# Optimization experiments

Hardware: AMD Instinct MI355X
Metric: run time of the kernel (lower is better)

The kernel has to match this reference:

```python
import jax, jax.numpy as jnp
import numpy as np

LEAKY = 0.5      # args.leaky
TEMP = 1.0       # args.temp
N_USER = 100000  # args.user
N_ITEM = 50000   # args.item
LATDIM = 128     # args.latdim
HYPERNUM = 128   # args.hyperNum
N_LAYERS = 2     # args.gnn_layer
N_EDGES = 1000000
BATCH = 4096


def _leaky(x):
    return jnp.maximum(LEAKY * x, x)


def _l2norm(x):
    # torch.nn.functional.normalize(p=2, dim=1): x / max(||x||, 1e-12)
    n = jnp.linalg.norm(x, axis=1, keepdims=True)
    return x / jnp.maximum(n, 1e-12)


def _spmm(rows, cols, vals, x, n_out):
    # torch.sparse.mm(adj, x) with adj given as COO (rows, cols, vals)
    return jax.ops.segment_sum(vals[:, None] * x[cols], rows, num_segments=n_out)


def _hyper_prop(lats, adj, Ws):
    # lats: [N, D], adj: [N, H] (dense hyper adjacency), Ws: [3, H, H]
    lat = _leaky(adj.T @ lats)                    # [H, D]
    for k in range(3):
        # (LeakyRelu(lat.T @ W)).T + lat == LeakyRelu(W.T @ lat) + lat
        lat = _leaky(Ws[k].T @ lat) + lat
    return _leaky(adj @ lat)                      # [N, D]


def _ssl(hyperLat, gnnLat):
    pos = jnp.exp(jnp.sum(hyperLat * gnnLat, axis=1) / TEMP)
    neg = jnp.sum(jnp.exp(gnnLat @ hyperLat.T / TEMP), axis=1)
    return jnp.sum(-jnp.log(pos / (neg + 1e-8) + 1e-8))


def setup_inputs() -> dict:
    key = jax.random.key(0)
    ks = jax.random.split(key, 12)
    # distinct ids so jnp.sort(ids) == torch.unique(ids)
    uids = jax.random.permutation(ks[0], N_USER)[:BATCH].astype(jnp.int32)
    iids = jax.random.permutation(ks[1], N_ITEM)[:BATCH].astype(jnp.int32)
    adj_rows = jax.random.randint(ks[2], (N_EDGES,), 0, N_USER, dtype=jnp.int32)
    adj_cols = jax.random.randint(ks[3], (N_EDGES,), 0, N_ITEM, dtype=jnp.int32)
    adj_vals = jax.random.uniform(ks[4], (N_EDGES,), dtype=jnp.float32)
    s_emb = 0.05
    s_hh = (2.0 / (HYPERNUM + HYPERNUM)) ** 0.5   # xavier_normal
    s_dh = (2.0 / (LATDIM + HYPERNUM)) ** 0.5
    s_dd = (2.0 / (LATDIM + LATDIM)) ** 0.5
    uEmbed0 = jax.random.normal(ks[5], (N_USER, LATDIM), jnp.float32) * s_emb
    iEmbed0 = jax.random.normal(ks[6], (N_ITEM, LATDIM), jnp.float32) * s_emb
    uhyper = jax.random.normal(ks[7], (LATDIM, HYPERNUM), jnp.float32) * s_dh
    ihyper = jax.random.normal(ks[8], (LATDIM, HYPERNUM), jnp.float32) * s_dh
    Wu = jax.random.normal(ks[9], (N_LAYERS, 3, HYPERNUM, HYPERNUM), jnp.float32) * s_hh
    Wi = jax.random.normal(ks[10], (N_LAYERS, 3, HYPERNUM, HYPERNUM), jnp.float32) * s_hh
    Wt = jax.random.normal(ks[11], (N_LAYERS, LATDIM, LATDIM), jnp.float32) * s_dd
    return {"uids": uids, "iids": iids, "adj_rows": adj_rows, "adj_cols": adj_cols,
            "adj_vals": adj_vals, "uEmbed0": uEmbed0, "iEmbed0": iEmbed0,
            "uhyper": uhyper, "ihyper": ihyper, "Wu": Wu, "Wi": Wi, "Wt": Wt}


def reference(uids, iids, adj_rows, adj_cols, adj_vals, uEmbed0, iEmbed0,
              uhyper, ihyper, Wu, Wi, Wt):
    # droprate = 0 => edgeDropout and feature dropout are identity
    uuHyper = uEmbed0 @ uhyper   # [N_USER, H]
    iiHyper = iEmbed0 @ ihyper   # [N_ITEM, H]
    ulats, ilats = [uEmbed0], [iEmbed0]
    gnnU, gnnI, hypU, hypI = [], [], [], []
    for l in range(N_LAYERS):
        ulat = _leaky(_spmm(adj_rows, adj_cols, adj_vals, ilats[-1], N_USER))
        ilat = _leaky(_spmm(adj_cols, adj_rows, adj_vals, ulats[-1], N_ITEM))
        hu = _hyper_prop(ulats[-1], uuHyper, Wu[l])
        hi = _hyper_prop(ilats[-1], iiHyper, Wi[l])
        gnnU.append(ulat); gnnI.append(ilat); hypU.append(hu); hypI.append(hi)
        ulats.append(ulat + hu + ulats[-1])
        ilats.append(ilat + hi + ilats[-1])
    ulat = sum(ulats)
    ilat = sum(ilats)
    preds = jnp.sum(ulat[uids] * ilat[iids], axis=-1)
    uniqU = jnp.sort(uids)  # uids are distinct -> equals torch.unique
    uniqI = jnp.sort(iids)
    ssl = jnp.asarray(0.0, jnp.float32)
    for l in range(N_LAYERS):
        ssl = ssl + _ssl(_l2norm(hypU[l][uniqU]) @ Wt[l], _l2norm(gnnU[l][uniqU]))
        ssl = ssl + _ssl(_l2norm(hypI[l][uniqI]) @ Wt[l], _l2norm(gnnI[l][uniqI]))
    reg = (jnp.sum(jnp.square(uEmbed0)) + jnp.sum(jnp.square(iEmbed0)) +
           jnp.sum(jnp.square(uhyper)) + jnp.sum(jnp.square(ihyper)))
    return preds, ssl, reg
```

## Files before the change

### kernel.cpp

```cpp
#include <hip/hip_runtime.h>

#define NU 100000
#define NI 50000
#define DD 128
#define HH 128
#define NE 1000000
#define NB 4096
#define SCHUNK 2048
#define ATBB 512

__device__ __forceinline__ float lk(float x) { return fmaxf(0.5f * x, x); }

__global__ __launch_bounds__(256) void hist_kernel(const int* __restrict__ idx,
                                                   int* __restrict__ deg, int n) {
  int e = blockIdx.x * 256 + threadIdx.x;
  if (e < n) atomicAdd(&deg[idx[e]], 1);
}

__global__ __launch_bounds__(256) void scan_bsum(const int* __restrict__ deg,
                                                 int* __restrict__ bsum, int N) {
  int b = blockIdx.x, t = threadIdx.x;
  int base = b * SCHUNK;
  int s = 0;
  for (int i = t; i < SCHUNK; i += 256) {
    int g = base + i;
    if (g < N) s += deg[g];
  }
#pragma unroll
  for (int o = 32; o > 0; o >>= 1) s += __shfl_down(s, o);
  __shared__ int ws[4];
  if ((t & 63) == 0) ws[t >> 6] = s;
  __syncthreads();
  if (t == 0) bsum[b] = ws[0] + ws[1] + ws[2] + ws[3];
}

__global__ __launch_bounds__(256) void scan_top(int* __restrict__ bsum, int G) {
  int t = threadIdx.x;
  __shared__ int sh[256];
  int v = (t < G) ? bsum[t] : 0;
  sh[t] = v;
  __syncthreads();
  for (int o = 1; o < 256; o <<= 1) {
    int add = (t >= o) ? sh[t - o] : 0;
    __syncthreads();
    sh[t] += add;
    __syncthreads();
  }
  if (t < G) bsum[t] = sh[t] - v;
}

__global__ __launch_bounds__(256) void scan_write(const int* __restrict__ deg,
                                                  const int* __restrict__ bsumx,
                                                  int* __restrict__ rowptr,
                                                  int* __restrict__ cursor,
                                                  int N, int total) {
  int b = blockIdx.x, t = threadIdx.x;
  int base = b * SCHUNK + t * 8;
  int v[8], s = 0;
#pragma unroll
  for (int i = 0; i < 8; i++) {
    int g = base + i;
    v[i] = (g < N) ? deg[g] : 0;
    s += v[i];
  }
  __shared__ int sh[256];
  sh[t] = s;
  __syncthreads();
  for (int o = 1; o < 256; o <<= 1) {
    int add = (t >= o) ? sh[t - o] : 0;
    __syncthreads();
    sh[t] += add;
    __syncthreads();
  }
  int off = bsumx[b] + sh[t] - s;
#pragma unroll
  for (int i = 0; i < 8; i++) {
    int g = base + i;
    if (g < N) { rowptr[g] = off; cursor[g] = off; }
    off += v[i];
  }
  if (b == 0 && t == 0) rowptr[N] = total;
}

__global__ __launch_bounds__(256) void scatter_kernel(const int* __restrict__ idx,
                                                      const int* __restrict__ other,
                                                      const float* __restrict__ vals,
                                                      int* __restrict__ cursor,
                                                      int* __restrict__ scol,
                                                      float* __restrict__ sval, int n) {
  int e = blockIdx.x * 256 + threadIdx.x;
  if (e < n) {
    int p = atomicAdd(&cursor[idx[e]], 1);
    scol[p] = other[e];
    sval[p] = vals[e];
  }
}

__global__ __launch_bounds__(256) void spmm_csr_kernel(
    const int* __restrict__ rowptr, const int* __restrict__ scol,
    const float* __restrict__ sval, const float* __restrict__ x,
    float* __restrict__ y, int N) {
  int w = (blockIdx.x * 256 + threadIdx.x) >> 6;
  if (w >= N) return;
  int lane = threadIdx.x & 63;
  int half = lane >> 5, l32 = lane & 31;
  const float4* x4 = (const float4*)x;
  int j0 = rowptr[w], j1 = rowptr[w + 1];
  float ax = 0.f, ay = 0.f, az = 0.f, aw = 0.f;
  int j = j0 + half;
  for (; j + 2 < j1; j += 4) {
    int c0 = scol[j], c1 = scol[j + 2];
    float v0 = sval[j], v1 = sval[j + 2];
    float4 x0 = x4[(size_t)c0 * 32 + l32];
    float4 x1 = x4[(size_t)c1 * 32 + l32];
    ax += v0 * x0.x + v1 * x1.x;
    ay += v0 * x0.y + v1 * x1.y;
    az += v0 * x0.z + v1 * x1.z;
    aw += v0 * x0.w + v1 * x1.w;
  }
  for (; j < j1; j += 2) {
    int c0 = scol[j];
    float v0 = sval[j];
    float4 x0 = x4[(size_t)c0 * 32 + l32];
    ax += v0 * x0.x; ay += v0 * x0.y; az += v0 * x0.z; aw += v0 * x0.w;
  }
  ax += __shfl_xor(ax, 32); ay += __shfl_xor(ay, 32);
  az += __shfl_xor(az, 32); aw += __shfl_xor(aw, 32);
  if (half == 0) {
    float4 r; r.x = ax; r.y = ay; r.z = az; r.w = aw;
    ((float4*)y)[(size_t)w * 32 + l32] = r;
  }
}

__global__ __launch_bounds__(256) void atb_kernel(
    const float* __restrict__ E, const float* __restrict__ X,
    float* __restrict__ part, int N) {
  __shared__ __align__(16) float Es[64][132];
  __shared__ __align__(16) float Xs[64][132];
  int t = threadIdx.x;
  int ip = (t >> 4) << 2;
  int jp = (t & 15) << 2;
  int rpb = (N + (int)gridDim.x - 1) / (int)gridDim.x;
  int n0 = blockIdx.x * rpb;
  int n1 = min(n0 + rpb, N);
  float acc[2][2][4][4] = {};
  const float4* E4 = (const float4*)E;
  const float4* X4 = (const float4*)X;
  for (int n = n0; n < n1; n += 64) {
    int nr = min(64, n1 - n);
    __syncthreads();
#pragma unroll
    for (int q = 0; q < 8; q++) {
      int f = t + (q << 8);
      int row = f >> 5, c4 = f & 31;
      float4 ev = {0.f, 0.f, 0.f, 0.f}, xv = {0.f, 0.f, 0.f, 0.f};
      if (row < nr) {
        size_t gi = (size_t)(n + row) * 32 + c4;
        ev = E4[gi]; xv = X4[gi];
      }
      *(float4*)&Es[row][c4 << 2] = ev;
      *(float4*)&Xs[row][c4 << 2] = xv;
    }
    __syncthreads();
#pragma unroll 2
    for (int rr = 0; rr < 64; rr++) {
      float4 e0 = *(const float4*)&Es[rr][ip];
      float4 e1 = *(const float4*)&Es[rr][ip + 64];
      float4 x0 = *(const float4*)&Xs[rr][jp];
      float4 x1 = *(const float4*)&Xs[rr][jp + 64];
      const float* e0p = (const float*)&e0;
      const float* e1p = (const float*)&e1;
      const float* x0p = (const float*)&x0;
      const float* x1p = (const float*)&x1;
#pragma unroll
      for (int ai = 0; ai < 4; ai++)
#pragma unroll
        for (int aj = 0; aj < 4; aj++) {
          acc[0][0][ai][aj] += e0p[ai] * x0p[aj];
          acc[0][1][ai][aj] += e0p[ai] * x1p[aj];
          acc[1][0][ai][aj] += e1p[ai] * x0p[aj];
          acc[1][1][ai][aj] += e1p[ai] * x1p[aj];
        }
    }
  }
  float* dst = part + (size_t)blockIdx.x * 16384;
#pragma unroll
  for (int rh = 0; rh < 2; rh++)
#pragma unroll
    for (int ai = 0; ai < 4; ai++) {
      int row = rh * 64 + ip + ai;
#pragma unroll
      for (int ch = 0; ch < 2; ch++) {
        float4 v;
        v.x = acc[rh][ch][ai][0]; v.y = acc[rh][ch][ai][1];
        v.z = acc[rh][ch][ai][2]; v.w = acc[rh][ch][ai][3];
        *(float4*)&dst[row * 128 + ch * 64 + jp] = v;
      }
    }
}

__global__ __launch_bounds__(256) void reduce_atb_kernel(
    const float* __restrict__ part, float* __restrict__ A) {
  int e4 = blockIdx.x * 256 + threadIdx.x;
  const float4* p4 = (const float4*)part;
  float4 s = {0.f, 0.f, 0.f, 0.f};
#pragma unroll 4
  for (int b = 0; b < ATBB; b++) {
    float4 v = p4[(size_t)b * 4096 + e4];
    s.x += v.x; s.y += v.y; s.z += v.z; s.w += v.w;
  }
  ((float4*)A)[e4] = s;
}

__global__ __launch_bounds__(256) void chain_kernel(
    const float* __restrict__ A_u, const float* __restrict__ A_i,
    const float* __restrict__ uhy, const float* __restrict__ ihy,
    const float* __restrict__ Wu_l, const float* __restrict__ Wi_l,
    float* __restrict__ B_u, float* __restrict__ B_i) {
  __shared__ float Wb[128 * 132];
  __shared__ float LA[128][16];
  __shared__ float LB[128][16];
  int side = blockIdx.x >> 3, strip = blockIdx.x & 7;
  const float* A = side ? A_i : A_u;
  const float* hy = side ? ihy : uhy;
  const float* W = side ? Wi_l : Wu_l;
  float* Bo = side ? B_i : B_u;
  int t = threadIdx.x;
  int j0 = strip * 16;
  for (int i = t; i < 2048; i += 256) LA[i >> 4][i & 15] = A[(i >> 4) * 128 + j0 + (i & 15)];
  for (int i = t; i < 16384; i += 256) Wb[(i >> 7) * 132 + (i & 127)] = hy[i];
  __syncthreads();
  int jc = t & 15, i0 = (t >> 4) * 8;
  {
    float acc[8] = {};
    for (int k = 0; k < 128; k++) {
      float lv = LA[k][jc];
      const float* wr = &Wb[k * 132 + i0];
#pragma unroll
      for (int a = 0; a < 8; a++) acc[a] += wr[a] * lv;
    }
#pragma unroll
    for (int a = 0; a < 8; a++) LB[i0 + a][jc] = lk(acc[a]);
  }
  __syncthreads();
  float (*pin)[16] = LB;
  float (*pout)[16] = LA;
  for (int s = 0; s < 3; s++) {
    for (int i = t; i < 16384; i += 256) Wb[(i >> 7) * 132 + (i & 127)] = W[s * 16384 + i];
    __syncthreads();
    float acc[8] = {};
    for (int k = 0; k < 128; k++) {
      float lv = pin[k][jc];
      const float* wr = &Wb[k * 132 + i0];
#pragma unroll
      for (int a = 0; a < 8; a++) acc[a] += wr[a] * lv;
    }
#pragma unroll
    for (int a = 0; a < 8; a++) pout[i0 + a][jc] = lk(acc[a]) + pin[i0 + a][jc];
    __syncthreads();
    float (*tmp)[16] = pin; pin = pout; pout = tmp;
  }
  for (int i = t; i < 16384; i += 256) Wb[(i >> 7) * 132 + (i & 127)] = hy[i];
  __syncthreads();
  {
    int i = t >> 1, jb = (t & 1) * 8;
    float acc[8] = {};
    for (int k = 0; k < 128; k++) {
      float hv = Wb[i * 132 + k];
      const float* lr = &pin[k][jb];
#pragma unroll
      for (int b = 0; b < 8; b++) acc[b] += hv * lr[b];
    }
#pragma unroll
    for (int b = 0; b < 8; b++) Bo[i * 128 + j0 + jb + b] = acc[b];
  }
}

__global__ __launch_bounds__(512) void nmul_upd_kernel(
    const float* __restrict__ E, const float* __restrict__ Bm,
    const float* __restrict__ gnn, float* __restrict__ cur, int N) {
  __shared__ __align__(16) float Bs[128][128];
  int t = threadIdx.x;
  int dg = t & 15, rg = t >> 4;
  const float4* B4 = (const float4*)Bm;
#pragma unroll
  for (int q = 0; q < 8; q++) {
    int f = t + (q << 9);
    *(float4*)&Bs[f >> 5][(f & 31) << 2] = B4[f];
  }
  __syncthreads();
  int n0 = blockIdx.x << 7;
  const float4* E4 = (const float4*)E;
  float acc[4][8] = {};
  int rows[4];
  bool val[4];
#pragma unroll
  for (int a = 0; a < 4; a++) { rows[a] = n0 + rg + (a << 5); val[a] = rows[a] < N; }
  for (int h4 = 0; h4 < 128; h4 += 4) {
    float4 ev[4];
#pragma unroll
    for (int a = 0; a < 4; a++)
      ev[a] = val[a] ? E4[(size_t)rows[a] * 32 + (h4 >> 2)]
                     : make_float4(0.f, 0.f, 0.f, 0.f);
#pragma unroll
    for (int hh = 0; hh < 4; hh++) {
      float4 b0 = *(const float4*)&Bs[h4 + hh][dg << 2];
      float4 b1 = *(const float4*)&Bs[h4 + hh][(dg << 2) + 64];
#pragma unroll
      for (int a = 0; a < 4; a++) {
        float e = ((const float*)&ev[a])[hh];
        acc[a][0] += e * b0.x; acc[a][1] += e * b0.y;
        acc[a][2] += e * b0.z; acc[a][3] += e * b0.w;
        acc[a][4] += e * b1.x; acc[a][5] += e * b1.y;
        acc[a][6] += e * b1.z; acc[a][7] += e * b1.w;
      }
    }
  }
#pragma unroll
  for (int a = 0; a < 4; a++) {
    if (val[a]) {
      size_t base = (size_t)rows[a] * DD + (dg << 2);
      float4 g0 = *(const float4*)(gnn + base);
      float4 g1 = *(const float4*)(gnn + base + 64);
      float4 c0 = *(const float4*)(cur + base);
      float4 c1 = *(const float4*)(cur + base + 64);
      c0.x += lk(g0.x) + lk(acc[a][0]); c0.y += lk(g0.y) + lk(acc[a][1]);
      c0.z += lk(g0.z) + lk(acc[a][2]); c0.w += lk(g0.w) + lk(acc[a][3]);
      c1.x += lk(g1.x) + lk(acc[a][4]); c1.y += lk(g1.y) + lk(acc[a][5]);
      c1.z += lk(g1.z) + lk(acc[a][6]); c1.w += lk(g1.w) + lk(acc[a][7]);
      *(float4*)(cur + base) = c0; *(float4*)(cur + base + 64) = c1;
    }
  }
}

__global__ __launch_bounds__(128) void sslgath_kernel(
    const int* __restrict__ ids, const float* __restrict__ gnn,
    const float* __restrict__ E, const float* __restrict__ Bm,
    float* __restrict__ og, float* __restrict__ oh) {
  __shared__ __align__(16) float Bs[128][132];
  __shared__ __align__(16) float Eb[32][132];
  __shared__ int idb[32];
  int t = threadIdx.x;
  int base = blockIdx.x * 32;
  if (t < 32) idb[t] = ids[base + t];
#pragma unroll
  for (int q = 0; q < 32; q++) {
    int f = t + q * 128;
    *(float4*)&Bs[f >> 5][(f & 31) << 2] = ((const float4*)Bm)[f];
  }
  __syncthreads();
#pragma unroll
  for (int q = 0; q < 8; q++) {
    int f = t + q * 128;
    int r = f >> 5, c4 = f & 31;
    *(float4*)&Eb[r][c4 << 2] = ((const float4*)E)[(size_t)idb[r] * 32 + c4];
  }
  __syncthreads();
  float acc[32] = {};
  for (int k = 0; k < 128; k++) {
    float b = Bs[k][t];
#pragma unroll
    for (int r = 0; r < 32; r++) acc[r] += Eb[r][k] * b;
  }
  for (int r = 0; r < 32; r++) {
    int id = idb[r];
    og[(size_t)(base + r) * DD + t] = lk(gnn[(size_t)id * DD + t]);
    oh[(size_t)(base + r) * DD + t] = lk(acc[r]);
  }
}

__global__ __launch_bounds__(128) void gaccum_kernel(
    const int* __restrict__ ids, const float* __restrict__ cur,
    float* __restrict__ sumg) {
  int b = blockIdx.x, d = threadIdx.x;
  int id = ids[b];
  sumg[(size_t)b * DD + d] += cur[(size_t)id * DD + d];
}

__global__ __launch_bounds__(256) void preds_kernel(
    const float* __restrict__ su, const float* __restrict__ si,
    float* __restrict__ outp) {
  int gid = blockIdx.x * 256 + threadIdx.x;
  int w = gid >> 6, lane = gid & 63;
  if (w >= NB) return;
  float2 a = *(const float2*)(su + (size_t)w * DD + 2 * lane);
  float2 b = *(const float2*)(si + (size_t)w * DD + 2 * lane);
  float d = a.x * b.x + a.y * b.y;
#pragma unroll
  for (int o = 32; o > 0; o >>= 1) d += __shfl_down(d, o);
  if (lane == 0) outp[w] = d;
}

__global__ __launch_bounds__(256) void sumsq_kernel(
    const float* __restrict__ x, int n, float* __restrict__ outp) {
  float acc = 0.f;
  for (int i = blockIdx.x * 256 + threadIdx.x; i < n; i += gridDim.x * 256) {
    float v = x[i];
    acc += v * v;
  }
#pragma unroll
  for (int o = 32; o > 0; o >>= 1) acc += __shfl_down(acc, o);
  __shared__ float s[4];
  if ((threadIdx.x & 63) == 0) s[threadIdx.x >> 6] = acc;
  __syncthreads();
  if (threadIdx.x == 0) atomicAdd(outp, s[0] + s[1] + s[2] + s[3]);
}

__global__ __launch_bounds__(128) void norm_kernel(
    const float* __restrict__ gh, float* __restrict__ gg,
    float* __restrict__ hn) {
  int r = blockIdx.x, d = threadIdx.x;
  __shared__ float red[4];
  float hv = gh[(size_t)r * DD + d];
  float gv = gg[(size_t)r * DD + d];
  float h2 = hv * hv, g2 = gv * gv;
#pragma unroll
  for (int o = 32; o > 0; o >>= 1) { h2 += __shfl_down(h2, o); g2 += __shfl_down(g2, o); }
  if ((d & 63) == 0) { red[(d >> 6) * 2] = h2; red[(d >> 6) * 2 + 1] = g2; }
  __syncthreads();
  float hnorm = sqrtf(red[0] + red[2]);
  float gnorm = sqrtf(red[1] + red[3]);
  hn[(size_t)r * DD + d] = hv / fmaxf(hnorm, 1e-12f);
  gg[(size_t)r * DD + d] = gv / fmaxf(gnorm, 1e-12f);
}

__global__ __launch_bounds__(256) void nmul_plain_kernel(
    const float* __restrict__ In, const float* __restrict__ Wm,
    float* __restrict__ outp) {
  __shared__ __align__(16) float Bs[128][128];
  int t = threadIdx.x;
  int dg = t & 15, rg = t >> 4;
  const float4* W4 = (const float4*)Wm;
#pragma unroll
  for (int q = 0; q < 16; q++) {
    int f = t + (q << 8);
    *(float4*)&Bs[f >> 5][(f & 31) << 2] = W4[f];
  }
  __syncthreads();
  int n0 = blockIdx.x << 5;
  const float4* I4 = (const float4*)In;
  float acc[2][8] = {};
  for (int h4 = 0; h4 < 128; h4 += 4) {
    float4 ev[2];
#pragma unroll
    for (int a = 0; a < 2; a++)
      ev[a] = I4[(size_t)(n0 + rg + (a << 4)) * 32 + (h4 >> 2)];
#pragma unroll
    for (int hh = 0; hh < 4; hh++) {
      float4 b0 = *(const float4*)&Bs[h4 + hh][dg << 2];
      float4 b1 = *(const float4*)&Bs[h4 + hh][(dg << 2) + 64];
#pragma unroll
      for (int a = 0; a < 2; a++) {
        float e = ((const float*)&ev[a])[hh];
        acc[a][0] += e * b0.x; acc[a][1] += e * b0.y;
        acc[a][2] += e * b0.z; acc[a][3] += e * b0.w;
        acc[a][4] += e * b1.x; acc[a][5] += e * b1.y;
        acc[a][6] += e * b1.z; acc[a][7] += e * b1.w;
      }
    }
  }
#pragma unroll
  for (int a = 0; a < 2; a++) {
    size_t base = (size_t)(n0 + rg + (a << 4)) * DD + (dg << 2);
    float4 v0, v1;
    v0.x = acc[a][0]; v0.y = acc[a][1]; v0.z = acc[a][2]; v0.w = acc[a][3];
    v1.x = acc[a][4]; v1.y = acc[a][5]; v1.z = acc[a][6]; v1.w = acc[a][7];
    *(float4*)(outp + base) = v0;
    *(float4*)(outp + base + 64) = v1;
  }
}

__global__ __launch_bounds__(256) void gram_kernel(
    const float* __restrict__ gn, const float* __restrict__ hw,
    float* __restrict__ neg) {
  __shared__ __align__(16) float Hs[64][128];
  int t = threadIdx.x;
  int rg = t >> 4, dg = t & 15;
  int i0 = blockIdx.x << 7, j0 = blockIdx.y << 6;
  float4* Hs4 = (float4*)Hs;
  const float4* hw4 = (const float4*)hw;
#pragma unroll
  for (int q = 0; q < 8; q++) {
    int f = t + (q << 8);
    int j = f >> 5, k4 = f & 31;
    Hs4[j * 32 + (k4 ^ ((j >> 2) & 7))] = hw4[(size_t)(j0 + j) * 32 + k4];
  }
  __syncthreads();
  const float4* G4 = (const float4*)gn;
  float acc[8][4] = {};
  for (int h4 = 0; h4 < 128; h4 += 4) {
    int k4 = h4 >> 2;
    float4 gv[8];
#pragma unroll
    for (int a = 0; a < 8; a++)
      gv[a] = G4[(size_t)(i0 + rg + (a << 4)) * 32 + k4];
    float4 bv[4];
#pragma unroll
    for (int jj = 0; jj < 4; jj++) {
      int j = (dg << 2) + jj;
      bv[jj] = *(const float4*)&Hs[j][(k4 ^ ((j >> 2) & 7)) << 2];
    }
#pragma unroll
    for (int a = 0; a < 8; a++)
#pragma unroll
      for (int jj = 0; jj < 4; jj++)
        acc[a][jj] += gv[a].x * bv[jj].x + gv[a].y * bv[jj].y +
                      gv[a].z * bv[jj].z + gv[a].w * bv[jj].w;
  }
#pragma unroll
  for (int a = 0; a < 8; a++) {
    float s = expf(acc[a][0]) + expf(acc[a][1]) + expf(acc[a][2]) + expf(acc[a][3]);
    s += __shfl_xor(s, 1);
    s += __shfl_xor(s, 2);
    s += __shfl_xor(s, 4);
    s += __shfl_xor(s, 8);
    if (dg == 0) atomicAdd(&neg[i0 + rg + (a << 4)], s);
  }
}

__global__ __launch_bounds__(256) void sslfin_kernel(
    const float* __restrict__ gn, const float* __restrict__ hw,
    const float* __restrict__ neg, float* __restrict__ outp) {
  int gid = blockIdx.x * 256 + threadIdx.x;
  int w = gid >> 6, lane = gid & 63;
  if (w >= NB) return;
  float2 a = *(const float2*)(gn + (size_t)w * DD + 2 * lane);
  float2 b = *(const float2*)(hw + (size_t)w * DD + 2 * lane);
  float d = a.x * b.x + a.y * b.y;
#pragma unroll
  for (int o = 32; o > 0; o >>= 1) d += __shfl_down(d, o);
  if (lane == 0) {
    float pos = expf(d);
    float v = -logf(pos / (neg[w] + 1e-8f) + 1e-8f);
    atomicAdd(outp, v);
  }
}

extern "C" void kernel_launch(void* const* d_in, const int* in_sizes, int n_in,
                              void* d_out, int out_size, void* d_ws, size_t ws_size,
                              hipStream_t stream) {
  (void)in_sizes; (void)n_in; (void)out_size; (void)ws_size;
  const int* uids = (const int*)d_in[0];
  const int* iids = (const int*)d_in[1];
  const int* arow = (const int*)d_in[2];
  const int* acol = (const int*)d_in[3];
  const float* avals = (const float*)d_in[4];
  const float* uE = (const float*)d_in[5];
  const float* iE = (const float*)d_in[6];
  const float* uhy = (const float*)d_in[7];
  const float* ihy = (const float*)d_in[8];
  const float* Wu = (const float*)d_in[9];
  const float* Wi = (const float*)d_in[10];
  const float* Wt = (const float*)d_in[11];
  float* out = (float*)d_out;

  float* p = (float*)d_ws;
  float* cur_u = p; p += (size_t)NU * DD;
  float* gnn_u = p; p += (size_t)NU * DD;
  float* cur_i = p; p += (size_t)NI * DD;
  float* gnn_i = p; p += (size_t)NI * DD;
  float* A_u = p; p += HH * DD;
  float* A_i = p; p += HH * DD;
  float* B_u = p; p += HH * DD;
  float* B_i = p; p += HH * DD;
  float* sumg_u = p; p += (size_t)NB * DD;
  float* sumg_i = p; p += (size_t)NB * DD;
  float* region = p; p += (size_t)ATBB * 16384;
  float* negb = p; p += 4 * NB;
  int* rowptr_u = (int*)p; p += NU + 1;
  int* cursor_u = (int*)p; p += NU;
  int* rowptr_i = (int*)p; p += NI + 1;
  int* cursor_i = (int*)p; p += NI;
  int* bsum = (int*)p; p += 256;
  int* scol_u = (int*)p; p += NE;
  float* sval_u = p; p += NE;
  int* scol_i = (int*)p; p += NE;
  float* sval_i = p; p += NE;

  float* Apart = region;
  float* gg = region;
  float* gh = region + (size_t)NB * DD;
  float* hn = region + 2 * (size_t)NB * DD;

  const int GU = (NU + SCHUNK - 1) / SCHUNK;
  const int GI = (NI + SCHUNK - 1) / SCHUNK;
  const int EB = (NE + 255) / 256;
  const int TU = (NU + 127) >> 7;
  const int TI = (NI + 127) >> 7;

  hipMemsetAsync(cursor_u, 0, NU * sizeof(int), stream);
  hist_kernel<<<EB, 256, 0, stream>>>(arow, cursor_u, NE);
  scan_bsum<<<GU, 256, 0, stream>>>(cursor_u, bsum, NU);
  scan_top<<<1, 256, 0, stream>>>(bsum, GU);
  scan_write<<<GU, 256, 0, stream>>>(cursor_u, bsum, rowptr_u, cursor_u, NU, NE);
  scatter_kernel<<<EB, 256, 0, stream>>>(arow, acol, avals, cursor_u, scol_u, sval_u, NE);

  hipMemsetAsync(cursor_i, 0, NI * sizeof(int), stream);
  hist_kernel<<<EB, 256, 0, stream>>>(acol, cursor_i, NE);
  scan_bsum<<<GI, 256, 0, stream>>>(cursor_i, bsum, NI);
  scan_top<<<1, 256, 0, stream>>>(bsum, GI);
  scan_write<<<GI, 256, 0, stream>>>(cursor_i, bsum, rowptr_i, cursor_i, NI, NE);
  scatter_kernel<<<EB, 256, 0, stream>>>(acol, arow, avals, cursor_i, scol_i, sval_i, NE);

  hipMemcpyAsync(cur_u, uE, (size_t)NU * DD * 4, hipMemcpyDeviceToDevice, stream);
  hipMemcpyAsync(cur_i, iE, (size_t)NI * DD * 4, hipMemcpyDeviceToDevice, stream);
  hipMemsetAsync(out + NB, 0, 2 * sizeof(float), stream);
  hipMemsetAsync(negb, 0, 4 * NB * sizeof(float), stream);
  hipMemsetAsync(sumg_u, 0, 2 * (size_t)NB * DD * 4, stream);
  gaccum_kernel<<<NB, 128, 0, stream>>>(uids, uE, sumg_u);
  gaccum_kernel<<<NB, 128, 0, stream>>>(iids, iE, sumg_i);

  for (int l = 0; l < 2; l++) {
    const float* Wt_l = Wt + (size_t)l * DD * DD;
    spmm_csr_kernel<<<NU / 4, 256, 0, stream>>>(rowptr_u, scol_u, sval_u, cur_i, gnn_u, NU);
    spmm_csr_kernel<<<NI / 4, 256, 0, stream>>>(rowptr_i, scol_i, sval_i, cur_u, gnn_i, NI);
    atb_kernel<<<ATBB, 256, 0, stream>>>(uE, cur_u, Apart, NU);
    reduce_atb_kernel<<<16, 256, 0, stream>>>(Apart, A_u);
    atb_kernel<<<ATBB, 256, 0, stream>>>(iE, cur_i, Apart, NI);
    reduce_atb_kernel<<<16, 256, 0, stream>>>(Apart, A_i);
    chain_kernel<<<16, 256, 0, stream>>>(A_u, A_i, uhy, ihy,
        Wu + (size_t)l * 3 * HH * HH, Wi + (size_t)l * 3 * HH * HH, B_u, B_i);

    sslgath_kernel<<<NB / 32, 128, 0, stream>>>(uids, gnn_u, uE, B_u, gg, gh);
    nmul_upd_kernel<<<TU, 512, 0, stream>>>(uE, B_u, gnn_u, cur_u, NU);
    gaccum_kernel<<<NB, 128, 0, stream>>>(uids, cur_u, sumg_u);
    norm_kernel<<<NB, 128, 0, stream>>>(gh, gg, hn);
    nmul_plain_kernel<<<NB / 32, 256, 0, stream>>>(hn, Wt_l, gh);
    gram_kernel<<<dim3(NB / 128, NB / 64), 256, 0, stream>>>(gg, gh, negb + (2 * l) * NB);
    sslfin_kernel<<<NB / 4, 256, 0, stream>>>(gg, gh, negb + (2 * l) * NB, out + NB);

    sslgath_kernel<<<NB / 32, 128, 0, stream>>>(iids, gnn_i, iE, B_i, gg, gh);
    nmul_upd_kernel<<<TI, 512, 0, stream>>>(iE, B_i, gnn_i, cur_i, NI);
    gaccum_kernel<<<NB, 128, 0, stream>>>(iids, cur_i, sumg_i);
    norm_kernel<<<NB, 128, 0, stream>>>(gh, gg, hn);
    nmul_plain_kernel<<<NB / 32, 256, 0, stream>>>(hn, Wt_l, gh);
    gram_kernel<<<dim3(NB / 128, NB / 64), 256, 0, stream>>>(gg, gh, negb + (2 * l + 1) * NB);
    sslfin_kernel<<<NB / 4, 256, 0, stream>>>(gg, gh, negb + (2 * l + 1) * NB, out + NB);
  }

  preds_kernel<<<NB / 4, 256, 0, stream>>>(sumg_u, sumg_i, out);
  sumsq_kernel<<<2048, 256, 0, stream>>>(uE, NU * DD, out + NB + 1);
  sumsq_kernel<<<1024, 256, 0, stream>>>(iE, NI * DD, out + NB + 1);
  sumsq_kernel<<<64, 256, 0, stream>>>(uhy, DD * HH, out + NB + 1);
  sumsq_kernel<<<64, 256, 0, stream>>>(ihy, DD * HH, out + NB + 1);
}
```

Baseline: 2.217 ms.

## Merge user/item kernels and fuse hypergraph A^T X reduction into update pass

Batches the user and item variants of spmm, gather, gram, finalize, gaccum and sumsq into single launches indexed by side. The hyper-adjacency projection for layer 0 reads only the input embeddings, so it is computed once up front. The layer-1 projection is fused into the nmul update kernel's tile loop, which saves a separate read of the embeddings and current latents. The norm and Wt matmul kernels are merged. This removes many launches and some memory passes, at the cost of an extra synchronisation and serial per-row accumulation inside the update kernel.

```diff
diff --git a/kernel.cpp b/kernel.cpp
--- a/kernel.cpp
+++ b/kernel.cpp
@@ -7,7 +7,6 @@
 #define NE 1000000
 #define NB 4096
 #define SCHUNK 2048
-#define ATBB 512
 
 __device__ __forceinline__ float lk(float x) { return fmaxf(0.5f * x, x); }
 
@@ -96,11 +95,23 @@
   }
 }
 
-__global__ __launch_bounds__(256) void spmm_csr_kernel(
-    const int* __restrict__ rowptr, const int* __restrict__ scol,
-    const float* __restrict__ sval, const float* __restrict__ x,
-    float* __restrict__ y, int N) {
-  int w = (blockIdx.x * 256 + threadIdx.x) >> 6;
+__global__ __launch_bounds__(256) void spmm_both_kernel(
+    const int* __restrict__ rp_u, const int* __restrict__ sc_u,
+    const float* __restrict__ sv_u, const float* __restrict__ xu,
+    float* __restrict__ yu,
+    const int* __restrict__ rp_i, const int* __restrict__ sc_i,
+    const float* __restrict__ sv_i, const float* __restrict__ xi,
+    float* __restrict__ yi) {
+  int bid = blockIdx.x;
+  const int* rowptr; const int* scol; const float* sval;
+  const float* x; float* y; int N;
+  if (bid < NU / 4) {
+    rowptr = rp_u; scol = sc_u; sval = sv_u; x = xu; y = yu; N = NU;
+  } else {
+    bid -= NU / 4;
+    rowptr = rp_i; scol = sc_i; sval = sv_i; x = xi; y = yi; N = NI;
+  }
+  int w = bid * 4 + (threadIdx.x >> 6);
   if (w >= N) return;
   int lane = threadIdx.x & 63;
   int half = lane >> 5, l32 = lane & 31;
@@ -132,20 +143,20 @@
   }
 }
 
-__global__ __launch_bounds__(256) void atb_kernel(
-    const float* __restrict__ E, const float* __restrict__ X,
-    float* __restrict__ part, int N) {
+__global__ __launch_bounds__(256) void atb0_kernel(
+    const float* __restrict__ uE, const float* __restrict__ iE,
+    float* __restrict__ part) {
+  int side = blockIdx.x >> 8, bid = blockIdx.x & 255;
+  const float* E = side ? iE : uE;
+  int N = side ? NI : NU;
   __shared__ __align__(16) float Es[64][132];
-  __shared__ __align__(16) float Xs[64][132];
   int t = threadIdx.x;
-  int ip = (t >> 4) << 2;
-  int jp = (t & 15) << 2;
-  int rpb = (N + (int)gridDim.x - 1) / (int)gridDim.x;
-  int n0 = blockIdx.x * rpb;
+  int ip = (t >> 4) << 2, jp = (t & 15) << 2;
+  int rpb = (N + 255) >> 8;
+  int n0 = bid * rpb;
   int n1 = min(n0 + rpb, N);
   float acc[2][2][4][4] = {};
   const float4* E4 = (const float4*)E;
-  const float4* X4 = (const float4*)X;
   for (int n = n0; n < n1; n += 64) {
     int nr = min(64, n1 - n);
     __syncthreads();
@@ -153,21 +164,17 @@
     for (int q = 0; q < 8; q++) {
       int f = t + (q << 8);
       int row = f >> 5, c4 = f & 31;
-      float4 ev = {0.f, 0.f, 0.f, 0.f}, xv = {0.f, 0.f, 0.f, 0.f};
-      if (row < nr) {
-        size_t gi = (size_t)(n + row) * 32 + c4;
-        ev = E4[gi]; xv = X4[gi];
-      }
+      float4 ev = {0.f, 0.f, 0.f, 0.f};
+      if (row < nr) ev = E4[(size_t)(n + row) * 32 + c4];
       *(float4*)&Es[row][c4 << 2] = ev;
-      *(float4*)&Xs[row][c4 << 2] = xv;
     }
     __syncthreads();
 #pragma unroll 2
     for (int rr = 0; rr < 64; rr++) {
       float4 e0 = *(const float4*)&Es[rr][ip];
       float4 e1 = *(const float4*)&Es[rr][ip + 64];
-      float4 x0 = *(const float4*)&Xs[rr][jp];
-      float4 x1 = *(const float4*)&Xs[rr][jp + 64];
+      float4 x0 = *(const float4*)&Es[rr][jp];
+      float4 x1 = *(const float4*)&Es[rr][jp + 64];
       const float* e0p = (const float*)&e0;
       const float* e1p = (const float*)&e1;
       const float* x0p = (const float*)&x0;
@@ -199,17 +206,20 @@
     }
 }
 
-__global__ __launch_bounds__(256) void reduce_atb_kernel(
-    const float* __restrict__ part, float* __restrict__ A) {
-  int e4 = blockIdx.x * 256 + threadIdx.x;
-  const float4* p4 = (const float4*)part;
+__global__ __launch_bounds__(256) void reduce_both_kernel(
+    const float* __restrict__ part, float* __restrict__ A_u,
+    float* __restrict__ A_i) {
+  int b = blockIdx.x;
+  int side = b >> 4;
+  int e4 = (b & 15) * 256 + threadIdx.x;
+  const float4* p4 = (const float4*)(part + (size_t)side * 256 * 16384);
   float4 s = {0.f, 0.f, 0.f, 0.f};
 #pragma unroll 4
-  for (int b = 0; b < ATBB; b++) {
-    float4 v = p4[(size_t)b * 4096 + e4];
+  for (int k = 0; k < 256; k++) {
+    float4 v = p4[(size_t)k * 4096 + e4];
     s.x += v.x; s.y += v.y; s.z += v.z; s.w += v.w;
   }
-  ((float4*)A)[e4] = s;
+  ((float4*)(side ? A_i : A_u))[e4] = s;
 }
 
 __global__ __launch_bounds__(256) void chain_kernel(
@@ -276,9 +286,20 @@
   }
 }
 
-__global__ __launch_bounds__(512) void nmul_upd_kernel(
-    const float* __restrict__ E, const float* __restrict__ Bm,
-    const float* __restrict__ gnn, float* __restrict__ cur, int N) {
+template <int DOATB>
+__global__ __launch_bounds__(512) void nmul_atb_kernel(
+    const float* __restrict__ uE, const float* __restrict__ Bu,
+    const float* __restrict__ gu, float* __restrict__ cu,
+    const float* __restrict__ iE, const float* __restrict__ Bi,
+    const float* __restrict__ gi, float* __restrict__ ci,
+    float* __restrict__ part) {
+  int side = blockIdx.x >> 8, bid = blockIdx.x & 255;
+  const float* E = side ? iE : uE;
+  const float* Bm = side ? Bi : Bu;
+  const float* gnn = side ? gi : gu;
+  float* cur = side ? ci : cu;
+  int N = side ? NI : NU;
+  int ntiles = (N + 127) >> 7;
   __shared__ __align__(16) float Bs[128][128];
   int t = threadIdx.x;
   int dg = t & 15, rg = t >> 4;
@@ -289,54 +310,99 @@
     *(float4*)&Bs[f >> 5][(f & 31) << 2] = B4[f];
   }
   __syncthreads();
-  int n0 = blockIdx.x << 7;
+  float atb[4][8] = {};
   const float4* E4 = (const float4*)E;
-  float acc[4][8] = {};
-  int rows[4];
-  bool val[4];
-#pragma unroll
-  for (int a = 0; a < 4; a++) { rows[a] = n0 + rg + (a << 5); val[a] = rows[a] < N; }
-  for (int h4 = 0; h4 < 128; h4 += 4) {
-    float4 ev[4];
-#pragma unroll
-    for (int a = 0; a < 4; a++)
-      ev[a] = val[a] ? E4[(size_t)rows[a] * 32 + (h4 >> 2)]
-                     : make_float4(0.f, 0.f, 0.f, 0.f);
-#pragma unroll
-    for (int hh = 0; hh < 4; hh++) {
-      float4 b0 = *(const float4*)&Bs[h4 + hh][dg << 2];
-      float4 b1 = *(const float4*)&Bs[h4 + hh][(dg << 2) + 64];
-#pragma unroll
-      for (int a = 0; a < 4; a++) {
-        float e = ((const float*)&ev[a])[hh];
-        acc[a][0] += e * b0.x; acc[a][1] += e * b0.y;
-        acc[a][2] += e * b0.z; acc[a][3] += e * b0.w;
-        acc[a][4] += e * b1.x; acc[a][5] += e * b1.y;
-        acc[a][6] += e * b1.z; acc[a][7] += e * b1.w;
+  const float4* C4 = (const float4*)cur;
+  for (int tile = bid; tile < ntiles; tile += 256) {
+    int n0 = tile << 7;
+    float acc[4][8] = {};
+    int rows[4];
+    bool val[4];
+#pragma unroll
+    for (int a = 0; a < 4; a++) { rows[a] = n0 + rg + (a << 5); val[a] = rows[a] < N; }
+    for (int h4 = 0; h4 < 128; h4 += 4) {
+      float4 ev[4];
+#pragma unroll
+      for (int a = 0; a < 4; a++)
+        ev[a] = val[a] ? E4[(size_t)rows[a] * 32 + (h4 >> 2)]
+                       : make_float4(0.f, 0.f, 0.f, 0.f);
+#pragma unroll
+      for (int hh = 0; hh < 4; hh++) {
+        float4 b0 = *(const float4*)&Bs[h4 + hh][dg << 2];
+        float4 b1 = *(const float4*)&Bs[h4 + hh][(dg << 2) + 64];
+#pragma unroll
+        for (int a = 0; a < 4; a++) {
+          float e = ((const float*)&ev[a])[hh];
+          acc[a][0] += e * b0.x; acc[a][1] += e * b0.y;
+          acc[a][2] += e * b0.z; acc[a][3] += e * b0.w;
+          acc[a][4] += e * b1.x; acc[a][5] += e * b1.y;
+          acc[a][6] += e * b1.z; acc[a][7] += e * b1.w;
+        }
       }
     }
-  }
-#pragma unroll
-  for (int a = 0; a < 4; a++) {
-    if (val[a]) {
-      size_t base = (size_t)rows[a] * DD + (dg << 2);
-      float4 g0 = *(const float4*)(gnn + base);
-      float4 g1 = *(const float4*)(gnn + base + 64);
-      float4 c0 = *(const float4*)(cur + base);
-      float4 c1 = *(const float4*)(cur + base + 64);
-      c0.x += lk(g0.x) + lk(acc[a][0]); c0.y += lk(g0.y) + lk(acc[a][1]);
-      c0.z += lk(g0.z) + lk(acc[a][2]); c0.w += lk(g0.w) + lk(acc[a][3]);
-      c1.x += lk(g1.x) + lk(acc[a][4]); c1.y += lk(g1.y) + lk(acc[a][5]);
-      c1.z += lk(g1.z) + lk(acc[a][6]); c1.w += lk(g1.w) + lk(acc[a][7]);
-      *(float4*)(cur + base) = c0; *(float4*)(cur + base + 64) = c1;
-    }
-  }
-}
-
-__global__ __launch_bounds__(128) void sslgath_kernel(
-    const int* __restrict__ ids, const float* __restrict__ gnn,
-    const float* __restrict__ E, const float* __restrict__ Bm,
-    float* __restrict__ og, float* __restrict__ oh) {
+#pragma unroll
+    for (int a = 0; a < 4; a++) {
+      if (val[a]) {
+        size_t base = (size_t)rows[a] * DD + (dg << 2);
+        float4 g0 = *(const float4*)(gnn + base);
+        float4 g1 = *(const float4*)(gnn + base + 64);
+        float4 c0 = *(const float4*)(cur + base);
+        float4 c1 = *(const float4*)(cur + base + 64);
+        c0.x += lk(g0.x) + lk(acc[a][0]); c0.y += lk(g0.y) + lk(acc[a][1]);
+        c0.z += lk(g0.z) + lk(acc[a][2]); c0.w += lk(g0.w) + lk(acc[a][3]);
+        c1.x += lk(g1.x) + lk(acc[a][4]); c1.y += lk(g1.y) + lk(acc[a][5]);
+        c1.z += lk(g1.z) + lk(acc[a][6]); c1.w += lk(g1.w) + lk(acc[a][7]);
+        *(float4*)(cur + base) = c0; *(float4*)(cur + base + 64) = c1;
+      }
+    }
+    if (DOATB) {
+      __syncthreads();
+      int nr = min(128, N - n0);
+      for (int rr = 0; rr < nr; rr++) {
+        size_t rb = (size_t)(n0 + rr) * 32;
+        float4 ev = E4[rb + rg];
+        float4 c0 = C4[rb + (dg << 1)];
+        float4 c1 = C4[rb + (dg << 1) + 1];
+        const float* ep = (const float*)&ev;
+#pragma unroll
+        for (int ai = 0; ai < 4; ai++) {
+          float e = ep[ai];
+          atb[ai][0] += e * c0.x; atb[ai][1] += e * c0.y;
+          atb[ai][2] += e * c0.z; atb[ai][3] += e * c0.w;
+          atb[ai][4] += e * c1.x; atb[ai][5] += e * c1.y;
+          atb[ai][6] += e * c1.z; atb[ai][7] += e * c1.w;
+        }
+      }
+    }
+  }
+  if (DOATB) {
+    float* dst = part + (size_t)blockIdx.x * 16384;
+#pragma unroll
+    for (int ai = 0; ai < 4; ai++) {
+      int k = (rg << 2) + ai;
+      float4 v0, v1;
+      v0.x = atb[ai][0]; v0.y = atb[ai][1]; v0.z = atb[ai][2]; v0.w = atb[ai][3];
+      v1.x = atb[ai][4]; v1.y = atb[ai][5]; v1.z = atb[ai][6]; v1.w = atb[ai][7];
+      *(float4*)&dst[k * 128 + (dg << 3)] = v0;
+      *(float4*)&dst[k * 128 + (dg << 3) + 4] = v1;
+    }
+  }
+}
+
+__global__ __launch_bounds__(128) void sslgath_both_kernel(
+    const int* __restrict__ uids, const int* __restrict__ iids,
+    const float* __restrict__ gu, const float* __restrict__ gi,
+    const float* __restrict__ uE, const float* __restrict__ iE,
+    const float* __restrict__ Bu, const float* __restrict__ Bi,
+    float* __restrict__ ggu, float* __restrict__ ghu,
+    float* __restrict__ ggi, float* __restrict__ ghi) {
+  int side = blockIdx.y;
+  const int* ids = side ? iids : uids;
+  const float* gnn = side ? gi : gu;
+  const float* E = side ? iE : uE;
+  const float* Bm = side ? Bi : Bu;
+  float* og = side ? ggi : ggu;
+  float* oh = side ? ghi : ghu;
   __shared__ __align__(16) float Bs[128][132];
   __shared__ __align__(16) float Eb[32][132];
   __shared__ int idb[32];
@@ -369,9 +435,14 @@
   }
 }
 
-__global__ __launch_bounds__(128) void gaccum_kernel(
-    const int* __restrict__ ids, const float* __restrict__ cur,
-    float* __restrict__ sumg) {
+__global__ __launch_bounds__(128) void gaccum_both_kernel(
+    const int* __restrict__ uids, const int* __restrict__ iids,
+    const float* __restrict__ cu, const float* __restrict__ ci,
+    float* __restrict__ su, float* __restrict__ si) {
+  int side = blockIdx.y;
+  const int* ids = side ? iids : uids;
+  const float* cur = side ? ci : cu;
+  float* sumg = side ? si : su;
   int b = blockIdx.x, d = threadIdx.x;
   int id = ids[b];
   sumg[(size_t)b * DD + d] += cur[(size_t)id * DD + d];
@@ -391,10 +462,18 @@
   if (lane == 0) outp[w] = d;
 }
 
-__global__ __launch_bounds__(256) void sumsq_kernel(
-    const float* __restrict__ x, int n, float* __restrict__ outp) {
+__global__ __launch_bounds__(256) void sumsq4_kernel(
+    const float* __restrict__ uE, const float* __restrict__ iE,
+    const float* __restrict__ uhy, const float* __restrict__ ihy,
+    float* __restrict__ outp) {
+  int b = blockIdx.x;
+  const float* x; int n, base, nb;
+  if (b < 2048) { x = uE; n = NU * DD; base = b; nb = 2048; }
+  else if (b < 3072) { x = iE; n = NI * DD; base = b - 2048; nb = 1024; }
+  else if (b < 3136) { x = uhy; n = DD * HH; base = b - 3072; nb = 64; }
+  else { x = ihy; n = DD * HH; base = b - 3136; nb = 64; }
   float acc = 0.f;
-  for (int i = blockIdx.x * 256 + threadIdx.x; i < n; i += gridDim.x * 256) {
+  for (int i = base * 256 + threadIdx.x; i < n; i += nb * 256) {
     float v = x[i];
     acc += v * v;
   }
@@ -406,73 +485,105 @@
   if (threadIdx.x == 0) atomicAdd(outp, s[0] + s[1] + s[2] + s[3]);
 }
 
-__global__ __launch_bounds__(128) void norm_kernel(
-    const float* __restrict__ gh, float* __restrict__ gg,
-    float* __restrict__ hn) {
-  int r = blockIdx.x, d = threadIdx.x;
-  __shared__ float red[4];
-  float hv = gh[(size_t)r * DD + d];
-  float gv = gg[(size_t)r * DD + d];
-  float h2 = hv * hv, g2 = gv * gv;
-#pragma unroll
-  for (int o = 32; o > 0; o >>= 1) { h2 += __shfl_down(h2, o); g2 += __shfl_down(g2, o); }
-  if ((d & 63) == 0) { red[(d >> 6) * 2] = h2; red[(d >> 6) * 2 + 1] = g2; }
-  __syncthreads();
-  float hnorm = sqrtf(red[0] + red[2]);
-  float gnorm = sqrtf(red[1] + red[3]);
-  hn[(size_t)r * DD + d] = hv / fmaxf(hnorm, 1e-12f);
-  gg[(size_t)r * DD + d] = gv / fmaxf(gnorm, 1e-12f);
-}
-
-__global__ __launch_bounds__(256) void nmul_plain_kernel(
-    const float* __restrict__ In, const float* __restrict__ Wm,
-    float* __restrict__ outp) {
-  __shared__ __align__(16) float Bs[128][128];
+__global__ __launch_bounds__(256) void normplain_kernel(
+    float* __restrict__ ggu, float* __restrict__ ghu,
+    float* __restrict__ ggi, float* __restrict__ ghi,
+    const float* __restrict__ Wt_l) {
+  int side = blockIdx.x >> 7, bid = blockIdx.x & 127;
+  float* gg = side ? ggi : ggu;
+  float* gh = side ? ghi : ghu;
+  __shared__ __align__(16) float Ws[128][128];
+  __shared__ __align__(16) float Gh[32][132];
+  __shared__ __align__(16) float Gg[32][132];
+  __shared__ float red[32][8][2];
+  __shared__ float inv[32][2];
   int t = threadIdx.x;
-  int dg = t & 15, rg = t >> 4;
-  const float4* W4 = (const float4*)Wm;
+  const float4* W4 = (const float4*)Wt_l;
 #pragma unroll
   for (int q = 0; q < 16; q++) {
     int f = t + (q << 8);
-    *(float4*)&Bs[f >> 5][(f & 31) << 2] = W4[f];
-  }
-  __syncthreads();
-  int n0 = blockIdx.x << 5;
-  const float4* I4 = (const float4*)In;
+    *(float4*)&Ws[f >> 5][(f & 31) << 2] = W4[f];
+  }
+  int n0 = bid << 5;
+  const float4* gh4 = (const float4*)gh;
+  const float4* gg4 = (const float4*)gg;
+#pragma unroll
+  for (int q = 0; q < 4; q++) {
+    int f = t + (q << 8);
+    int r = f >> 5, c4 = f & 31;
+    *(float4*)&Gh[r][c4 << 2] = gh4[(size_t)(n0 + r) * 32 + c4];
+    *(float4*)&Gg[r][c4 << 2] = gg4[(size_t)(n0 + r) * 32 + c4];
+  }
+  __syncthreads();
+  {
+    int r = t >> 3, seg = t & 7;
+    float sh = 0.f, sg = 0.f;
+    int k0 = seg << 4;
+#pragma unroll
+    for (int k = 0; k < 16; k++) {
+      float a = Gh[r][k0 + k]; sh += a * a;
+      float b = Gg[r][k0 + k]; sg += b * b;
+    }
+    red[r][seg][0] = sh; red[r][seg][1] = sg;
+  }
+  __syncthreads();
+  if (t < 64) {
+    int r = t >> 1, which = t & 1;
+    float s = 0.f;
+#pragma unroll
+    for (int seg = 0; seg < 8; seg++) s += red[r][seg][which];
+    inv[r][which] = 1.f / fmaxf(sqrtf(s), 1e-12f);
+  }
+  __syncthreads();
+  float4* ggw = (float4*)gg;
+#pragma unroll
+  for (int q = 0; q < 4; q++) {
+    int f = t + (q << 8);
+    int r = f >> 5, c4 = f & 31;
+    float4 v = *(const float4*)&Gg[r][c4 << 2];
+    float iv = inv[r][1];
+    v.x *= iv; v.y *= iv; v.z *= iv; v.w *= iv;
+    ggw[(size_t)(n0 + r) * 32 + c4] = v;
+  }
+  int rg = t >> 4, dg = t & 15;
   float acc[2][8] = {};
-  for (int h4 = 0; h4 < 128; h4 += 4) {
-    float4 ev[2];
-#pragma unroll
-    for (int a = 0; a < 2; a++)
-      ev[a] = I4[(size_t)(n0 + rg + (a << 4)) * 32 + (h4 >> 2)];
-#pragma unroll
-    for (int hh = 0; hh < 4; hh++) {
-      float4 b0 = *(const float4*)&Bs[h4 + hh][dg << 2];
-      float4 b1 = *(const float4*)&Bs[h4 + hh][(dg << 2) + 64];
-#pragma unroll
-      for (int a = 0; a < 2; a++) {
-        float e = ((const float*)&ev[a])[hh];
-        acc[a][0] += e * b0.x; acc[a][1] += e * b0.y;
-        acc[a][2] += e * b0.z; acc[a][3] += e * b0.w;
-        acc[a][4] += e * b1.x; acc[a][5] += e * b1.y;
-        acc[a][6] += e * b1.z; acc[a][7] += e * b1.w;
-      }
-    }
+  for (int k = 0; k < 128; k++) {
+    float e0 = Gh[rg][k];
+    float e1 = Gh[rg + 16][k];
+    float4 b0 = *(const float4*)&Ws[k][dg << 2];
+    float4 b1 = *(const float4*)&Ws[k][(dg << 2) + 64];
+    acc[0][0] += e0 * b0.x; acc[0][1] += e0 * b0.y;
+    acc[0][2] += e0 * b0.z; acc[0][3] += e0 * b0.w;
+    acc[0][4] += e0 * b1.x; acc[0][5] += e0 * b1.y;
+    acc[0][6] += e0 * b1.z; acc[0][7] += e0 * b1.w;
+    acc[1][0] += e1 * b0.x; acc[1][1] += e1 * b0.y;
+    acc[1][2] += e1 * b0.z; acc[1][3] += e1 * b0.w;
+    acc[1][4] += e1 * b1.x; acc[1][5] += e1 * b1.y;
+    acc[1][6] += e1 * b1.z; acc[1][7] += e1 * b1.w;
   }
 #pragma unroll
   for (int a = 0; a < 2; a++) {
-    size_t base = (size_t)(n0 + rg + (a << 4)) * DD + (dg << 2);
+    int r = rg + (a << 4);
+    float iv = inv[r][0];
+    size_t base = (size_t)(n0 + r) * DD + (dg << 2);
     float4 v0, v1;
-    v0.x = acc[a][0]; v0.y = acc[a][1]; v0.z = acc[a][2]; v0.w = acc[a][3];
-    v1.x = acc[a][4]; v1.y = acc[a][5]; v1.z = acc[a][6]; v1.w = acc[a][7];
-    *(float4*)(outp + base) = v0;
-    *(float4*)(outp + base + 64) = v1;
-  }
-}
-
-__global__ __launch_bounds__(256) void gram_kernel(
-    const float* __restrict__ gn, const float* __restrict__ hw,
-    float* __restrict__ neg) {
+    v0.x = acc[a][0] * iv; v0.y = acc[a][1] * iv;
+    v0.z = acc[a][2] * iv; v0.w = acc[a][3] * iv;
+    v1.x = acc[a][4] * iv; v1.y = acc[a][5] * iv;
+    v1.z = acc[a][6] * iv; v1.w = acc[a][7] * iv;
+    *(float4*)(gh + base) = v0;
+    *(float4*)(gh + base + 64) = v1;
+  }
+}
+
+__global__ __launch_bounds__(256) void gram_both_kernel(
+    const float* __restrict__ ggu, const float* __restrict__ ghu,
+    const float* __restrict__ ggi, const float* __restrict__ ghi,
+    float* __restrict__ negl) {
+  int side = blockIdx.z;
+  const float* gn = side ? ggi : ggu;
+  const float* hw = side ? ghi : ghu;
+  float* neg = negl + side * NB;
   __shared__ __align__(16) float Hs[64][128];
   int t = threadIdx.x;
   int rg = t >> 4, dg = t & 15;
@@ -518,9 +629,14 @@
   }
 }
 
-__global__ __launch_bounds__(256) void sslfin_kernel(
-    const float* __restrict__ gn, const float* __restrict__ hw,
-    const float* __restrict__ neg, float* __restrict__ outp) {
+__global__ __launch_bounds__(256) void sslfin_both_kernel(
+    const float* __restrict__ ggu, const float* __restrict__ ghu,
+    const float* __restrict__ ggi, const float* __restrict__ ghi,
+    const float* __restrict__ negl, float* __restrict__ outp) {
+  int side = blockIdx.y;
+  const float* gn = side ? ggi : ggu;
+  const float* hw = side ? ghi : ghu;
+  const float* neg = negl + side * NB;
   int gid = blockIdx.x * 256 + threadIdx.x;
   int w = gid >> 6, lane = gid & 63;
   if (w >= NB) return;
@@ -565,7 +681,11 @@
   float* B_i = p; p += HH * DD;
   float* sumg_u = p; p += (size_t)NB * DD;
   float* sumg_i = p; p += (size_t)NB * DD;
-  float* region = p; p += (size_t)ATBB * 16384;
+  float* Apart = p; p += (size_t)512 * 16384;
+  float* ggu = p; p += (size_t)NB * DD;
+  float* ghu = p; p += (size_t)NB * DD;
+  float* ggi = p; p += (size_t)NB * DD;
+  float* ghi = p; p += (size_t)NB * DD;
   float* negb = p; p += 4 * NB;
   int* rowptr_u = (int*)p; p += NU + 1;
   int* cursor_u = (int*)p; p += NU;
@@ -577,16 +697,9 @@
   int* scol_i = (int*)p; p += NE;
   float* sval_i = p; p += NE;
 
-  float* Apart = region;
-  float* gg = region;
-  float* gh = region + (size_t)NB * DD;
-  float* hn = region + 2 * (size_t)NB * DD;
-
   const int GU = (NU + SCHUNK - 1) / SCHUNK;
   const int GI = (NI + SCHUNK - 1) / SCHUNK;
   const int EB = (NE + 255) / 256;
-  const int TU = (NU + 127) >> 7;
-  const int TI = (NI + 127) >> 7;
 
   hipMemsetAsync(cursor_u, 0, NU * sizeof(int), stream);
   hist_kernel<<<EB, 256, 0, stream>>>(arow, cursor_u, NE);
@@ -607,40 +720,37 @@
   hipMemsetAsync(out + NB, 0, 2 * sizeof(float), stream);
   hipMemsetAsync(negb, 0, 4 * NB * sizeof(float), stream);
   hipMemsetAsync(sumg_u, 0, 2 * (size_t)NB * DD * 4, stream);
-  gaccum_kernel<<<NB, 128, 0, stream>>>(uids, uE, sumg_u);
-  gaccum_kernel<<<NB, 128, 0, stream>>>(iids, iE, sumg_i);
+  gaccum_both_kernel<<<dim3(NB, 2), 128, 0, stream>>>(uids, iids, uE, iE, sumg_u, sumg_i);
+
+  atb0_kernel<<<512, 256, 0, stream>>>(uE, iE, Apart);
+  reduce_both_kernel<<<32, 256, 0, stream>>>(Apart, A_u, A_i);
 
   for (int l = 0; l < 2; l++) {
     const float* Wt_l = Wt + (size_t)l * DD * DD;
-    spmm_csr_kernel<<<NU / 4, 256, 0, stream>>>(rowptr_u, scol_u, sval_u, cur_i, gnn_u, NU);
-    spmm_csr_kernel<<<NI / 4, 256, 0, stream>>>(rowptr_i, scol_i, sval_i, cur_u, gnn_i, NI);
-    atb_kernel<<<ATBB, 256, 0, stream>>>(uE, cur_u, Apart, NU);
-    reduce_atb_kernel<<<16, 256, 0, stream>>>(Apart, A_u);
-    atb_kernel<<<ATBB, 256, 0, stream>>>(iE, cur_i, Apart, NI);
-    reduce_atb_kernel<<<16, 256, 0, stream>>>(Apart, A_i);
+    spmm_both_kernel<<<NU / 4 + NI / 4, 256, 0, stream>>>(
+        rowptr_u, scol_u, sval_u, cur_i, gnn_u,
+        rowptr_i, scol_i, sval_i, cur_u, gnn_i);
     chain_kernel<<<16, 256, 0, stream>>>(A_u, A_i, uhy, ihy,
         Wu + (size_t)l * 3 * HH * HH, Wi + (size_t)l * 3 * HH * HH, B_u, B_i);
-
-    sslgath_kernel<<<NB / 32, 128, 0, stream>>>(uids, gnn_u, uE, B_u, gg, gh);
-    nmul_upd_kernel<<<TU, 512, 0, stream>>>(uE, B_u, gnn_u, cur_u, NU);
-    gaccum_kernel<<<NB, 128, 0, stream>>>(uids, cur_u, sumg_u);
-    norm_kernel<<<NB, 128, 0, stream>>>(gh, gg, hn);
-    nmul_plain_kernel<<<NB / 32, 256, 0, stream>>>(hn, Wt_l, gh);
-    gram_kernel<<<dim3(NB / 128, NB / 64), 256, 0, stream>>>(gg, gh, negb + (2 * l) * NB);
-    sslfin_kernel<<<NB / 4, 256, 0, stream>>>(gg, gh, negb + (2 * l) * NB, out + NB);
-
-    sslgath_kernel<<<NB / 32, 128, 0, stream>>>(iids, gnn_i, iE, B_i, gg, gh);
-    nmul_upd_kernel<<<TI, 512, 0, stream>>>(iE, B_i, gnn_i, cur_i, NI);
-    gaccum_kernel<<<NB, 128, 0, stream>>>(iids, cur_i, sumg_i);
-    norm_kernel<<<NB, 128, 0, stream>>>(gh, gg, hn);
-    nmul_plain_kernel<<<NB / 32, 256, 0, stream>>>(hn, Wt_l, gh);
-    gram_kernel<<<dim3(NB / 128, NB / 64), 256, 0, stream>>>(gg, gh, negb + (2 * l + 1) * NB);
-    sslfin_kernel<<<NB / 4, 256, 0, stream>>>(gg, gh, negb + (2 * l + 1) * NB, out + NB);
+    sslgath_both_kernel<<<dim3(NB / 32, 2), 128, 0, stream>>>(
+        uids, iids, gnn_u, gnn_i, uE, iE, B_u, B_i, ggu, ghu, ggi, ghi);
+    if (l == 0) {
+      nmul_atb_kernel<1><<<512, 512, 0, stream>>>(uE, B_u, gnn_u, cur_u,
+                                                  iE, B_i, gnn_i, cur_i, Apart);
+      reduce_both_kernel<<<32, 256, 0, stream>>>(Apart, A_u, A_i);
+    } else {
+      nmul_atb_kernel<0><<<512, 512, 0, stream>>>(uE, B_u, gnn_u, cur_u,
+                                                  iE, B_i, gnn_i, cur_i, nullptr);
+    }
+    gaccum_both_kernel<<<dim3(NB, 2), 128, 0, stream>>>(uids, iids, cur_u, cur_i,
+                                                        sumg_u, sumg_i);
+    normplain_kernel<<<256, 256, 0, stream>>>(ggu, ghu, ggi, ghi, Wt_l);
+    gram_both_kernel<<<dim3(NB / 128, NB / 64, 2), 256, 0, stream>>>(
+        ggu, ghu, ggi, ghi, negb + 2 * l * NB);
+    sslfin_both_kernel<<<dim3(NB / 4, 2), 256, 0, stream>>>(
+        ggu, ghu, ggi, ghi, negb + 2 * l * NB, out + NB);
   }
 
   preds_kernel<<<NB / 4, 256, 0, stream>>>(sumg_u, sumg_i, out);
-  sumsq_kernel<<<2048, 256, 0, stream>>>(uE, NU * DD, out + NB + 1);
-  sumsq_kernel<<<1024, 256, 0, stream>>>(iE, NI * DD, out + NB + 1);
-  sumsq_kernel<<<64, 256, 0, stream>>>(uhy, DD * HH, out + NB + 1);
-  sumsq_kernel<<<64, 256, 0, stream>>>(ihy, DD * HH, out + NB + 1);
-}
+  sumsq4_kernel<<<3200, 256, 0, stream>>>(uE, iE, uhy, ihy, out + NB + 1);
+}
```

Result: faster. 2.102 ms (-5.2%).
